# Kernel optimization log

Hardware: AMD Instinct MI355X
Metric: run time of the kernel (lower is better)

The kernel has to match this reference:

```python
import jax, jax.numpy as jnp
import numpy as np

B, C_IN, C_OUT, W_DIM = 4, 512, 512, 512
H = W = 84
K = 3
UP = DOWN = 2
TAPS = 12          # filter_size(6) * up_factor(2)
PAD_LO, PAD_HI = 9, 8
SLOPE = 0.2
GAIN = float(np.sqrt(2.0))
CLAMP = 256.0
AFF_GAIN = 1.0 / float(np.sqrt(W_DIM))  # FullyConnectedLayer weight_gain


def _kaiser_beta(a):
    if a > 50:
        return 0.1102 * (a - 8.7)
    if a > 21:
        return 0.5842 * (a - 21.0) ** 0.4 + 0.07886 * (a - 21.0)
    return 0.0


def _design_lowpass(numtaps, cutoff, width, fs):
    # replicates scipy.signal.firwin(numtaps, cutoff, width=width, fs=fs)
    nyq = 0.5 * fs
    atten = 2.285 * (numtaps - 1) * np.pi * (width / nyq) + 7.95
    beta = _kaiser_beta(atten)
    m = np.arange(numtaps) - (numtaps - 1) / 2.0
    c = cutoff / nyq
    h = c * np.sinc(c * m)
    n = np.arange(numtaps)
    win = np.i0(beta * np.sqrt(np.clip(1.0 - (2.0 * n / (numtaps - 1) - 1.0) ** 2, 0.0, 1.0))) / np.i0(beta)
    h = h * win
    h = h / h.sum()
    return jnp.asarray(h, dtype=jnp.float32)


# tmp_sampling_rate = 128; in/out cutoff = 16, half_width = 8 -> width = 16
FU = _design_lowpass(TAPS, 16.0, 16.0, 128.0)
FD = _design_lowpass(TAPS, 16.0, 16.0, 128.0)


def _dwconv(x, f1d, axis, stride=1, dilation=1, pad=(0, 0)):
    # depthwise conv of NCHW x with a 1-D filter along spatial `axis` (2=H, 3=W)
    C = x.shape[1]
    if axis == 2:
        k = jnp.tile(f1d.reshape(1, 1, -1, 1), (C, 1, 1, 1))
        strides, ld, padding = (stride, 1), (dilation, 1), (pad, (0, 0))
    else:
        k = jnp.tile(f1d.reshape(1, 1, 1, -1), (C, 1, 1, 1))
        strides, ld, padding = (1, stride), (1, dilation), ((0, 0), pad)
    return jax.lax.conv_general_dilated(x, k, window_strides=strides, padding=padding,
                                        lhs_dilation=ld,
                                        dimension_numbers=('NCHW', 'OIHW', 'NCHW'),
                                        feature_group_count=C)


def setup_inputs():
    key = jax.random.key(0)
    ks = jax.random.split(key, 5)
    return {
        'x': jax.random.normal(ks[0], (B, C_IN, H, W), jnp.float32),
        'w_latent': jax.random.normal(ks[1], (B, W_DIM), jnp.float32),
        'aff_w': jax.random.normal(ks[2], (C_IN, W_DIM), jnp.float32),
        'aff_b': jnp.ones((C_IN,), jnp.float32),  # bias_init=1
        'conv_w': jax.random.normal(ks[3], (C_OUT, C_IN, K, K), jnp.float32),
        'conv_b': jax.random.normal(ks[4], (C_OUT,), jnp.float32) * 0.1,
    }


def reference(x, w_latent, aff_w, aff_b, conv_w, conv_b):
    # --- style affine (FullyConnectedLayer, linear activation) ---
    s = w_latent @ (aff_w * AFF_GAIN).T + aff_b  # [B, C_IN]
    # --- modulated conv2d with demodulation, folded into input/output scaling ---
    wn = conv_w * jax.lax.rsqrt(jnp.mean(conv_w * conv_w, axis=(1, 2, 3), keepdims=True))
    sn = s * jax.lax.rsqrt(jnp.mean(s * s))
    w2 = jnp.sum(wn * wn, axis=(2, 3))                    # [O, I]
    dcoef = jax.lax.rsqrt((sn * sn) @ w2.T + 1e-8)        # [B, O]
    input_gain = 1.0  # magnitude_ema == 1 -> rsqrt(ema) == 1
    xm = x * (sn * input_gain)[:, :, None, None]
    y = jax.lax.conv_general_dilated(xm, wn, window_strides=(1, 1),
                                     padding=((K - 1, K - 1), (K - 1, K - 1)),
                                     dimension_numbers=('NCHW', 'OIHW', 'NCHW'))
    y = y * dcoef[:, :, None, None]
    # --- filtered leaky-relu: bias -> up-FIR(gain up^2) -> lrelu*sqrt(2), clamp -> FIR-down ---
    y = y + conv_b[None, :, None, None]
    fu = (FU * UP)[::-1]  # total gain up^2 split over the two separable passes; flipped for conv
    y = _dwconv(y, fu, axis=2, dilation=UP, pad=(PAD_LO, PAD_HI + UP - 1))
    y = _dwconv(y, fu, axis=3, dilation=UP, pad=(PAD_LO, PAD_HI + UP - 1))
    y = jnp.where(y < 0, y * SLOPE, y) * GAIN
    y = jnp.clip(y, -CLAMP, CLAMP)
    fd = FD[::-1]
    y = _dwconv(y, fd, axis=2, stride=DOWN)
    y = _dwconv(y, fd, axis=3, stride=DOWN)
    return y  # [B, C_OUT, 84, 84]
```

## Files before the change

kernel.cpp:

```cpp
#include <hip/hip_runtime.h>
#include <hip/hip_bf16.h>
#include <math.h>

typedef __attribute__((ext_vector_type(8))) short bf16x8;
typedef __attribute__((ext_vector_type(4))) float f32x4;

#define B_    4
#define C_    512
#define HW_   84
#define HP_   86
#define XP_   88
#define NPIX  (HP_*HP_)
#define XPIX  (XP_*XP_)
#define YSEG  ((size_t)2048 * NPIX)

struct Taps { float fu[12]; float fd[12]; };

__device__ __forceinline__ unsigned short f2bf(float f) {
    unsigned int u = __float_as_uint(f);
    unsigned int r = (u + 0x7fffu + ((u >> 16) & 1u)) >> 16;
    return (unsigned short)r;
}
__device__ __forceinline__ float bf2f(unsigned short u) {
    return __uint_as_float((unsigned int)u << 16);
}
__device__ __forceinline__ void gload_lds16(const unsigned short* g, unsigned short* l) {
    __builtin_amdgcn_global_load_lds((const __attribute__((address_space(1))) void*)g,
                                     (__attribute__((address_space(3))) void*)l, 16, 0, 0);
}

__global__ __launch_bounds__(256) void k_prep(const float* __restrict__ wlat,
                                              const float* __restrict__ aff_w,
                                              const float* __restrict__ aff_b,
                                              const float* __restrict__ conv_w,
                                              float* __restrict__ s_raw,
                                              float* __restrict__ parts,
                                              unsigned short* __restrict__ wn3,
                                              float* __restrict__ w2) {
    __shared__ float red[256];
    __shared__ float wlds[4608];
    int tid = threadIdx.x;
    if (blockIdx.x < 512) {
        int wv = tid >> 6, lane = tid & 63;
        int w = blockIdx.x * 4 + wv;
        int b = w >> 9, c = w & 511;
        const float4* aw = (const float4*)(aff_w + (size_t)c * 512);
        const float4* wl = (const float4*)(wlat + b * 512);
        float4 a0 = aw[lane * 2], a1 = aw[lane * 2 + 1];
        float4 w0 = wl[lane * 2], w1 = wl[lane * 2 + 1];
        float acc = a0.x * w0.x + a0.y * w0.y + a0.z * w0.z + a0.w * w0.w
                  + a1.x * w1.x + a1.y * w1.y + a1.z * w1.z + a1.w * w1.w;
        #pragma unroll
        for (int m = 1; m < 64; m <<= 1) acc += __shfl_xor(acc, m, 64);
        if (lane == 0) {
            float s = acc * 0.04419417382415922f + aff_b[c];
            s_raw[w] = s; red[wv] = s * s;
        }
        __syncthreads();
        if (tid == 0) parts[blockIdx.x] = red[0] + red[1] + red[2] + red[3];
    } else {
        int o = blockIdx.x - 512;
        const float* wo = conv_w + (size_t)o * 4608;
        float ss = 0.f;
        for (int i = tid; i < 4608; i += 256) { float v = wo[i]; wlds[i] = v; ss += v * v; }
        red[tid] = ss; __syncthreads();
        for (int off = 128; off > 0; off >>= 1) {
            if (tid < off) red[tid] += red[tid + off];
            __syncthreads();
        }
        float scale = rsqrtf(red[0] / 4608.f);
        int og = o >> 5, o32 = o & 31;
        for (int c = tid; c < 512; c += 256) {
            float s2 = 0.f;
            #pragma unroll
            for (int k = 0; k < 9; k++) { float v = wlds[c * 9 + k] * scale; s2 += v * v; }
            w2[(size_t)o * 512 + c] = s2;
        }
        for (int idx = tid; idx < 4608; idx += 256) {
            int cc = idx / 288, rem = idx - cc * 288;
            int kk = rem >> 5, c32 = rem & 31;
            float v = wlds[(cc * 32 + c32) * 9 + kk] * scale;
            wn3[(((size_t)cc * 16 + og) * 32 + o32) * 288 + rem] = f2bf(v);
        }
    }
}

__global__ __launch_bounds__(256) void k_moddc(const float* __restrict__ s_raw,
                                               const float* __restrict__ parts,
                                               const float* __restrict__ w2,
                                               const float* __restrict__ x,
                                               float* __restrict__ dcoef,
                                               unsigned short* __restrict__ xpad2) {
    int lane = threadIdx.x & 63;
    const float4* pp = (const float4*)parts;
    float4 p0 = pp[lane * 2], p1 = pp[lane * 2 + 1];
    float tot = p0.x + p0.y + p0.z + p0.w + p1.x + p1.y + p1.z + p1.w;
    #pragma unroll
    for (int m = 1; m < 64; m <<= 1) tot += __shfl_xor(tot, m, 64);
    float inv = rsqrtf(tot / 2048.f);

    if (blockIdx.x >= 512) {
        int wv = threadIdx.x >> 6;
        int w = (blockIdx.x - 512) * 4 + wv;
        int b = w >> 9, o = w & 511;
        const float4* sr = (const float4*)(s_raw + b * 512);
        const float4* wr = (const float4*)(w2 + (size_t)o * 512);
        float acc = 0.f;
        #pragma unroll
        for (int q = 0; q < 2; q++) {
            float4 s = sr[lane * 2 + q], ww = wr[lane * 2 + q];
            float s0 = s.x * inv, s1 = s.y * inv, s2 = s.z * inv, s3 = s.w * inv;
            acc += ww.x * s0 * s0 + ww.y * s1 * s1 + ww.z * s2 * s2 + ww.w * s3 * s3;
        }
        #pragma unroll
        for (int m = 1; m < 64; m <<= 1) acc += __shfl_xor(acc, m, 64);
        if (lane == 0) dcoef[w] = rsqrtf(acc + 1e-8f);
    } else {
        int pb = blockIdx.x;
        int b = pb >> 7; int rem = pb & 127;
        int cg = rem >> 1, half = rem & 1;
        float sv[8];
        #pragma unroll
        for (int e = 0; e < 8; e++) sv[e] = s_raw[b * 512 + cg * 8 + e] * inv;
        const float* xbase = x + ((size_t)(b * 512 + cg * 8)) * (HW_ * HW_);
        unsigned short* op = xpad2 + ((size_t)(b * 64 + cg)) * XPIX * 8;
        int pr0 = half * (XPIX / 4), pr1 = pr0 + XPIX / 4;
        for (int pr = pr0 + threadIdx.x; pr < pr1; pr += 256) {
            int r = pr / 44, q = pr - r * 44;
            uint4 d0, d1;
            if (r >= 2 && r < 86 && q >= 1 && q <= 42) {
                int off = (r - 2) * HW_ + 2 * q - 2;
                unsigned int w0[4], w1[4];
                #pragma unroll
                for (int e = 0; e < 4; e++) {
                    float2 fa = *(const float2*)(xbase + (size_t)(2 * e) * (HW_ * HW_) + off);
                    float2 fb = *(const float2*)(xbase + (size_t)(2 * e + 1) * (HW_ * HW_) + off);
                    w0[e] = (unsigned int)f2bf(fa.x * sv[2 * e]) | ((unsigned int)f2bf(fb.x * sv[2 * e + 1]) << 16);
                    w1[e] = (unsigned int)f2bf(fa.y * sv[2 * e]) | ((unsigned int)f2bf(fb.y * sv[2 * e + 1]) << 16);
                }
                d0.x = w0[0]; d0.y = w0[1]; d0.z = w0[2]; d0.w = w0[3];
                d1.x = w1[0]; d1.y = w1[1]; d1.z = w1[2]; d1.w = w1[3];
            } else {
                d0.x = d0.y = d0.z = d0.w = 0u;
                d1.x = d1.y = d1.z = d1.w = 0u;
            }
            *(uint4*)(op + (size_t)(2 * pr) * 8) = d0;
            *(uint4*)(op + (size_t)(2 * pr + 1) * 8) = d1;
        }
    }
}

__global__ __launch_bounds__(256, 3) void k_conv10(const unsigned short* __restrict__ xpad2,
                                                   const unsigned short* __restrict__ wn3,
                                                   const float* __restrict__ dcoef,
                                                   const float* __restrict__ conv_b,
                                                   unsigned short* __restrict__ ypart) {
    __shared__ __align__(16) unsigned short xs[2][4][384][8];

    int bid = blockIdx.x;
    int wg = (bid & 7) * 264 + (bid >> 3);
    int tile = wg % 66; int rest = wg / 66;
    int ot = rest & 3; int seg = (rest >> 2) & 1; int b = rest >> 3;

    int tid = threadIdx.x;
    int wv = tid >> 6, lane = tid & 63;
    int kgrp = lane >> 4, ln15 = lane & 15;
    int tr = tile / 6, tc = tile % 6;
    int r0 = tr * 8; if (r0 > 78) r0 = 78;
    int c0p = tc * 16; if (c0p > 70) c0p = 70;
    int og = ot * 4 + wv;

    const unsigned short* xseg = xpad2 + ((size_t)(b * 64 + seg * 32 + wv)) * XPIX * 8;
    int pA = lane, pB = 64 + lane, pC = (128 + lane > 179) ? 179 : 128 + lane;
    const unsigned short* gA = xseg + ((size_t)((r0 + pA / 18) * XP_ + c0p + pA % 18)) * 8;
    const unsigned short* gB = xseg + ((size_t)((r0 + pB / 18) * XP_ + c0p + pB % 18)) * 8;
    const unsigned short* gC = xseg + ((size_t)((r0 + pC / 18) * XP_ + c0p + pC % 18)) * 8;
    const size_t cstride = (size_t)4 * XPIX * 8;

    const unsigned short* wb0 = wn3 + (size_t)(seg * 8) * 147456 + ((size_t)(og * 32 + ln15)) * 288 + kgrp * 8;
    const unsigned short* wb1 = wb0 + (size_t)16 * 288;

    f32x4 acc[8][2];
    #pragma unroll
    for (int g = 0; g < 8; g++) { acc[g][0] = (f32x4){0,0,0,0}; acc[g][1] = (f32x4){0,0,0,0}; }

    gload_lds16(gA,           &xs[0][wv][0][0]);
    gload_lds16(gB,           &xs[0][wv][64][0]);
    gload_lds16(gC,           &xs[0][wv][128][0]);
    gload_lds16(gA + cstride, &xs[0][wv][192][0]);
    gload_lds16(gB + cstride, &xs[0][wv][256][0]);
    gload_lds16(gC + cstride, &xs[0][wv][320][0]);
    gA += 2 * cstride; gB += 2 * cstride; gC += 2 * cstride;
    __syncthreads();

    #pragma unroll 1
    for (int ph = 0; ph < 4; ++ph) {
        int cur = ph & 1, nb = cur ^ 1;
        if (ph < 3) {
            gload_lds16(gA, &xs[nb][wv][0][0]);
            gload_lds16(gB, &xs[nb][wv][64][0]);
            gload_lds16(gC, &xs[nb][wv][128][0]);
        }
        #pragma unroll
        for (int hf = 0; hf < 2; ++hf) {
            int pbase = hf * 192;
            #pragma unroll
            for (int kw = 0; kw < 3; ++kw) {
                bf16x8 F[10];
                #pragma unroll
                for (int r = 0; r < 10; ++r)
                    F[r] = *(const bf16x8*)&xs[cur][kgrp][pbase + r * 18 + ln15 + kw][0];
                #pragma unroll
                for (int kh = 0; kh < 3; ++kh) {
                    int kk = kh * 3 + kw;
                    bf16x8 W0 = *(const bf16x8*)(wb0 + kk * 32);
                    bf16x8 W1 = *(const bf16x8*)(wb1 + kk * 32);
                    __builtin_amdgcn_s_setprio(1);
                    #pragma unroll
                    for (int g = 0; g < 8; ++g) {
                        acc[g][0] = __builtin_amdgcn_mfma_f32_16x16x32_bf16(W0, F[g + kh], acc[g][0], 0, 0, 0);
                        acc[g][1] = __builtin_amdgcn_mfma_f32_16x16x32_bf16(W1, F[g + kh], acc[g][1], 0, 0, 0);
                    }
                    __builtin_amdgcn_s_setprio(0);
                }
            }
            wb0 += 147456; wb1 += 147456;
            if (hf == 0 && ph < 3) {
                gload_lds16(gA + cstride, &xs[nb][wv][192][0]);
                gload_lds16(gB + cstride, &xs[nb][wv][256][0]);
                gload_lds16(gC + cstride, &xs[nb][wv][320][0]);
                gA += 2 * cstride; gB += 2 * cstride; gC += 2 * cstride;
            }
        }
        __syncthreads();
    }

    float dcv[2][4], bvs[2][4];
    #pragma unroll
    for (int nt = 0; nt < 2; nt++)
        #pragma unroll
        for (int r = 0; r < 4; r++) {
            int o = og * 32 + nt * 16 + kgrp * 4 + r;
            dcv[nt][r] = dcoef[b * 512 + o];
            bvs[nt][r] = seg ? conv_b[o] : 0.f;
        }
    unsigned short* yp = ypart + (size_t)seg * YSEG;
    int pcol = c0p + ln15;
    #pragma unroll
    for (int g = 0; g < 8; ++g) {
        int prow = r0 + g;
        #pragma unroll
        for (int nt = 0; nt < 2; nt++)
            #pragma unroll
            for (int r = 0; r < 4; r++) {
                int o = og * 32 + nt * 16 + kgrp * 4 + r;
                yp[((size_t)(b * 512 + o)) * NPIX + prow * HP_ + pcol] =
                    f2bf(acc[g][nt][r] * dcv[nt][r] + bvs[nt][r]);
            }
    }
}

__global__ __launch_bounds__(512) void k_resample4(const unsigned short* __restrict__ ypart,
                                                   float* __restrict__ out, Taps taps) {
    __shared__ __align__(16) char smem[23760 + 25344];
    float (*yt)[96]            = (float(*)[96])smem;
    unsigned short (*upF)[180] = (unsigned short(*)[180])smem;
    float (*upR)[96]           = (float(*)[96])(smem + 23760);
    float (*dv)[180]           = (float(*)[180])(smem + 23760);

    int tid = threadIdx.x;
    int ts = blockIdx.x; int o = blockIdx.y; int b = blockIdx.z;
    int tr = ts * 28;
    const unsigned short* y0b = ypart + ((size_t)(b * 512 + o)) * NPIX;
    const unsigned short* y1b = y0b + YSEG;

    for (int idx = tid; idx < 38 * 94; idx += 512) {
        int rr = idx / 94, cc = idx % 94;
        int gr = tr - 4 + rr, gc = cc - 4;
        float v = 0.f;
        if (gr >= 0 && gr < HP_ && gc >= 0 && gc < HP_) {
            int p = gr * HP_ + gc;
            v = bf2f(y0b[p]) + bf2f(y1b[p]);
        }
        yt[rr][cc] = v;
    }
    __syncthreads();
    for (int idx = tid; idx < 11 * 94; idx += 512) {
        int ri = idx / 94, cc = idx % 94;
        int q0 = ri * 3;
        float w[8];
        #pragma unroll
        for (int u = 0; u < 8; u++) w[u] = yt[q0 + u][cc];
        #pragma unroll
        for (int j = 0; j < 3; j++) {
            float aE = 0.f, aO = 0.f;
            #pragma unroll
            for (int u = 0; u < 6; u++) {
                float v = w[j + u];
                aE += taps.fu[2 * u + 1] * v;
                aO += taps.fu[2 * u] * v;
            }
            upR[2 * (q0 + j)][cc] = aE;
            upR[2 * (q0 + j) + 1][cc] = aO;
        }
    }
    __syncthreads();
    for (int idx = tid; idx < 66 * 23; idx += 512) {
        int jr = idx / 23, rq = idx % 23;
        int q0 = rq * 4;
        int n = 89 - q0; if (n > 4) n = 4;
        float w[9];
        #pragma unroll
        for (int u = 0; u < 9; u++) w[u] = (u < n + 5) ? upR[jr][q0 + u] : 0.f;
        #pragma unroll
        for (int j = 0; j < 4; j++) {
            if (j < n) {
                float aE = 0.f, aO = 0.f;
                #pragma unroll
                for (int u = 0; u < 6; u++) {
                    float v = w[j + u];
                    aE += taps.fu[2 * u + 1] * v;
                    aO += taps.fu[2 * u] * v;
                }
                aE = (aE < 0.f ? aE * 0.2f : aE) * 1.4142135623730951f;
                aO = (aO < 0.f ? aO * 0.2f : aO) * 1.4142135623730951f;
                aE = fminf(fmaxf(aE, -256.f), 256.f);
                aO = fminf(fmaxf(aO, -256.f), 256.f);
                unsigned int pk = (unsigned int)f2bf(aE) | ((unsigned int)f2bf(aO) << 16);
                *(unsigned int*)&upF[jr][2 * (q0 + j)] = pk;
            }
        }
    }
    __syncthreads();
    for (int idx = tid; idx < 7 * 89; idx += 512) {
        int ri = idx / 89, jp = idx % 89;
        int ii0 = ri * 4;
        float lo[18], hi[18];
        #pragma unroll
        for (int t = 0; t < 18; t++) {
            unsigned int pk = *(const unsigned int*)&upF[2 * ii0 + t][2 * jp];
            lo[t] = bf2f((unsigned short)(pk & 0xffffu));
            hi[t] = bf2f((unsigned short)(pk >> 16));
        }
        #pragma unroll
        for (int j = 0; j < 4; j++) {
            float a0 = 0.f, a1 = 0.f;
            #pragma unroll
            for (int t = 0; t < 12; t++) {
                a0 += taps.fd[t] * lo[2 * j + t];
                a1 += taps.fd[t] * hi[2 * j + t];
            }
            *(float2*)&dv[ii0 + j][2 * jp] = make_float2(a0, a1);
        }
    }
    __syncthreads();
    for (int idx = tid; idx < 28 * 21; idx += 512) {
        int ii = idx / 21, rj = idx % 21;
        int jo0 = rj * 4;
        float w[18];
        const float2* dp = (const float2*)&dv[ii][2 * jo0];
        #pragma unroll
        for (int t = 0; t < 9; t++) {
            float2 d = dp[t];
            w[2 * t] = d.x; w[2 * t + 1] = d.y;
        }
        float4 res;
        #pragma unroll
        for (int j = 0; j < 4; j++) {
            float a = 0.f;
            #pragma unroll
            for (int t = 0; t < 12; t++) a += taps.fd[t] * w[2 * j + t];
            ((float*)&res)[j] = a;
        }
        *(float4*)&out[((size_t)(b * 512 + o) * 84 + (tr + ii)) * 84 + jo0] = res;
    }
}

static double bessel_i0(double x) {
    double s = 1.0, t = 1.0;
    for (int k = 1; k < 60; k++) {
        double u = x / (2.0 * k);
        t *= u * u;
        s += t;
        if (t < 1e-18 * s) break;
    }
    return s;
}

static void design_taps(float* h12) {
    const int N = 12;
    const double cutoff = 16.0, width = 16.0, fs = 128.0;
    double nyq = 0.5 * fs;
    double atten = 2.285 * (N - 1) * M_PI * (width / nyq) + 7.95;
    double beta;
    if (atten > 50.0) beta = 0.1102 * (atten - 8.7);
    else if (atten > 21.0) beta = 0.5842 * pow(atten - 21.0, 0.4) + 0.07886 * (atten - 21.0);
    else beta = 0.0;
    double c = cutoff / nyq;
    double h[12]; double sum = 0.0;
    double ib = bessel_i0(beta);
    for (int n = 0; n < N; n++) {
        double m = n - (N - 1) / 2.0;
        double xx = c * m;
        double sinc = (xx == 0.0) ? 1.0 : sin(M_PI * xx) / (M_PI * xx);
        double t = 2.0 * n / (N - 1) - 1.0;
        double arg = 1.0 - t * t; if (arg < 0.0) arg = 0.0;
        double w = bessel_i0(beta * sqrt(arg)) / ib;
        h[n] = c * sinc * w;
        sum += h[n];
    }
    for (int n = 0; n < N; n++) h12[n] = (float)(h[n] / sum);
}

extern "C" void kernel_launch(void* const* d_in, const int* in_sizes, int n_in,
                              void* d_out, int out_size, void* d_ws, size_t ws_size,
                              hipStream_t stream) {
    const float* x      = (const float*)d_in[0];
    const float* wlat   = (const float*)d_in[1];
    const float* aff_w  = (const float*)d_in[2];
    const float* aff_b  = (const float*)d_in[3];
    const float* conv_w = (const float*)d_in[4];
    const float* conv_b = (const float*)d_in[5];
    float* out = (float*)d_out;

    char* ws = (char*)d_ws;
    float* dcoef = (float*)ws + 2048;
    float* w2    = dcoef + 2048;
    unsigned short* wn3   = (unsigned short*)(w2 + 512 * 512);
    unsigned short* xpad2 = wn3 + (size_t)9 * 512 * 512;
    unsigned short* ypart = xpad2 + (size_t)B_ * 64 * XPIX * 8;
    float* s_raw = (float*)ypart;
    float* parts = s_raw + 2048;

    Taps taps;
    float h[12];
    design_taps(h);
    for (int t = 0; t < 12; t++) {
        taps.fu[t] = 2.0f * h[11 - t];
        taps.fd[t] = h[11 - t];
    }

    k_prep   <<<dim3(1024), dim3(256), 0, stream>>>(wlat, aff_w, aff_b, conv_w, s_raw, parts, wn3, w2);
    k_moddc  <<<dim3(1024), dim3(256), 0, stream>>>(s_raw, parts, w2, x, dcoef, xpad2);
    k_conv10 <<<dim3(2112), dim3(256), 0, stream>>>(xpad2, wn3, dcoef, conv_b, ypart);
    k_resample4<<<dim3(3, 512, 4), dim3(512), 0, stream>>>(ypart, out, taps);
}
```

Baseline: 253.1 us.

## Double output channels per wave in conv kernel to reuse LDS input fragments

Each wave now accumulates 64 output channels instead of 32, so every input fragment read from LDS feeds four MFMAs instead of two. This halves the number of blocks and the repeated staging of input tiles into LDS. Accumulator registers double and the occupancy hint drops from 3 to 2 blocks, which risks less latency hiding and more register pressure. The epilogue is also reordered to load each scale and bias once per channel.

Result: slower. 269.8 us (+6.6%).

```diff
diff --git a/kernel.cpp b/kernel.cpp
--- a/kernel.cpp
+++ b/kernel.cpp
@@ -150,7 +150,7 @@
     }
 }
 
-__global__ __launch_bounds__(256, 3) void k_conv10(const unsigned short* __restrict__ xpad2,
+__global__ __launch_bounds__(256, 2) void k_conv11(const unsigned short* __restrict__ xpad2,
                                                    const unsigned short* __restrict__ wn3,
                                                    const float* __restrict__ dcoef,
                                                    const float* __restrict__ conv_b,
@@ -158,9 +158,9 @@
     __shared__ __align__(16) unsigned short xs[2][4][384][8];
 
     int bid = blockIdx.x;
-    int wg = (bid & 7) * 264 + (bid >> 3);
+    int wg = (bid & 7) * 132 + (bid >> 3);
     int tile = wg % 66; int rest = wg / 66;
-    int ot = rest & 3; int seg = (rest >> 2) & 1; int b = rest >> 3;
+    int ot = rest & 1; int seg = (rest >> 1) & 1; int b = rest >> 2;
 
     int tid = threadIdx.x;
     int wv = tid >> 6, lane = tid & 63;
@@ -168,7 +168,6 @@
     int tr = tile / 6, tc = tile % 6;
     int r0 = tr * 8; if (r0 > 78) r0 = 78;
     int c0p = tc * 16; if (c0p > 70) c0p = 70;
-    int og = ot * 4 + wv;
 
     const unsigned short* xseg = xpad2 + ((size_t)(b * 64 + seg * 32 + wv)) * XPIX * 8;
     int pA = lane, pB = 64 + lane, pC = (128 + lane > 179) ? 179 : 128 + lane;
@@ -177,12 +176,18 @@
     const unsigned short* gC = xseg + ((size_t)((r0 + pC / 18) * XP_ + c0p + pC % 18)) * 8;
     const size_t cstride = (size_t)4 * XPIX * 8;
 
-    const unsigned short* wb0 = wn3 + (size_t)(seg * 8) * 147456 + ((size_t)(og * 32 + ln15)) * 288 + kgrp * 8;
+    int og2 = ot * 8 + wv * 2;
+    const unsigned short* wbase = wn3 + (size_t)(seg * 8) * 147456;
+    const unsigned short* wb0 = wbase + (size_t)og2 * 9216 + (size_t)ln15 * 288 + kgrp * 8;
     const unsigned short* wb1 = wb0 + (size_t)16 * 288;
-
-    f32x4 acc[8][2];
+    const unsigned short* wb2 = wbase + (size_t)(og2 + 1) * 9216 + (size_t)ln15 * 288 + kgrp * 8;
+    const unsigned short* wb3 = wb2 + (size_t)16 * 288;
+
+    f32x4 acc[8][4];
     #pragma unroll
-    for (int g = 0; g < 8; g++) { acc[g][0] = (f32x4){0,0,0,0}; acc[g][1] = (f32x4){0,0,0,0}; }
+    for (int g = 0; g < 8; g++)
+        #pragma unroll
+        for (int nt = 0; nt < 4; nt++) acc[g][nt] = (f32x4){0.f, 0.f, 0.f, 0.f};
 
     gload_lds16(gA,           &xs[0][wv][0][0]);
     gload_lds16(gB,           &xs[0][wv][64][0]);
@@ -215,16 +220,20 @@
                     int kk = kh * 3 + kw;
                     bf16x8 W0 = *(const bf16x8*)(wb0 + kk * 32);
                     bf16x8 W1 = *(const bf16x8*)(wb1 + kk * 32);
+                    bf16x8 W2 = *(const bf16x8*)(wb2 + kk * 32);
+                    bf16x8 W3 = *(const bf16x8*)(wb3 + kk * 32);
                     __builtin_amdgcn_s_setprio(1);
                     #pragma unroll
                     for (int g = 0; g < 8; ++g) {
                         acc[g][0] = __builtin_amdgcn_mfma_f32_16x16x32_bf16(W0, F[g + kh], acc[g][0], 0, 0, 0);
                         acc[g][1] = __builtin_amdgcn_mfma_f32_16x16x32_bf16(W1, F[g + kh], acc[g][1], 0, 0, 0);
+                        acc[g][2] = __builtin_amdgcn_mfma_f32_16x16x32_bf16(W2, F[g + kh], acc[g][2], 0, 0, 0);
+                        acc[g][3] = __builtin_amdgcn_mfma_f32_16x16x32_bf16(W3, F[g + kh], acc[g][3], 0, 0, 0);
                     }
                     __builtin_amdgcn_s_setprio(0);
                 }
             }
-            wb0 += 147456; wb1 += 147456;
+            wb0 += 147456; wb1 += 147456; wb2 += 147456; wb3 += 147456;
             if (hf == 0 && ph < 3) {
                 gload_lds16(gA + cstride, &xs[nb][wv][192][0]);
                 gload_lds16(gB + cstride, &xs[nb][wv][256][0]);
@@ -235,28 +244,20 @@
         __syncthreads();
     }
 
-    float dcv[2][4], bvs[2][4];
-    #pragma unroll
-    for (int nt = 0; nt < 2; nt++)
-        #pragma unroll
-        for (int r = 0; r < 4; r++) {
-            int o = og * 32 + nt * 16 + kgrp * 4 + r;
-            dcv[nt][r] = dcoef[b * 512 + o];
-            bvs[nt][r] = seg ? conv_b[o] : 0.f;
-        }
-    unsigned short* yp = ypart + (size_t)seg * YSEG;
+    unsigned short* yb = ypart + (size_t)seg * YSEG + ((size_t)b * 512) * NPIX;
     int pcol = c0p + ln15;
     #pragma unroll
-    for (int g = 0; g < 8; ++g) {
-        int prow = r0 + g;
-        #pragma unroll
-        for (int nt = 0; nt < 2; nt++)
-            #pragma unroll
-            for (int r = 0; r < 4; r++) {
-                int o = og * 32 + nt * 16 + kgrp * 4 + r;
-                yp[((size_t)(b * 512 + o)) * NPIX + prow * HP_ + pcol] =
-                    f2bf(acc[g][nt][r] * dcv[nt][r] + bvs[nt][r]);
-            }
+    for (int nt = 0; nt < 4; nt++) {
+        #pragma unroll
+        for (int r = 0; r < 4; r++) {
+            int o = ot * 256 + wv * 64 + nt * 16 + kgrp * 4 + r;
+            float dc = dcoef[b * 512 + o];
+            float bb = seg ? conv_b[o] : 0.f;
+            unsigned short* yo = yb + (size_t)o * NPIX + pcol;
+            #pragma unroll
+            for (int g = 0; g < 8; ++g)
+                yo[(r0 + g) * HP_] = f2bf(acc[g][nt][r] * dc + bb);
+        }
     }
 }
 
@@ -442,6 +443,6 @@
 
     k_prep   <<<dim3(1024), dim3(256), 0, stream>>>(wlat, aff_w, aff_b, conv_w, s_raw, parts, wn3, w2);
     k_moddc  <<<dim3(1024), dim3(256), 0, stream>>>(s_raw, parts, w2, x, dcoef, xpad2);
-    k_conv10 <<<dim3(2112), dim3(256), 0, stream>>>(xpad2, wn3, dcoef, conv_b, ypart);
+    k_conv11 <<<dim3(1056), dim3(256), 0, stream>>>(xpad2, wn3, dcoef, conv_b, ypart);
     k_resample4<<<dim3(3, 512, 4), dim3(512), 0, stream>>>(ypart, out, taps);
 }
```
